# Optimization experiments

Hardware: AMD Instinct MI355X
Metric: run time of the kernel (lower is better)

## Reference

```python
import jax, jax.numpy as jnp
import numpy as np

N_HEAD, D_MODEL, D_K, D_V = 8, 256, 32, 32
LN_EPS = 1e-5

def setup_inputs() -> dict:
    key = jax.random.key(0)
    ks = jax.random.split(key, 8)
    B, L = 2, 1024
    h = jax.random.normal(ks[0], (B, L, D_MODEL), dtype=jnp.float32)
    bias = jax.random.normal(ks[1], (B, L, L, D_K), dtype=jnp.float32) * 0.02
    std_qk = np.sqrt(2.0 / (D_MODEL + D_K)).astype(np.float32)
    std_v = np.sqrt(2.0 / (D_MODEL + D_V)).astype(np.float32)
    w_qs = jax.random.normal(ks[2], (N_HEAD * D_K, D_MODEL), dtype=jnp.float32) * std_qk
    w_ks = jax.random.normal(ks[3], (N_HEAD * D_K, D_MODEL), dtype=jnp.float32) * std_qk
    w_vs = jax.random.normal(ks[4], (N_HEAD * D_V, D_MODEL), dtype=jnp.float32) * std_v
    ln_g = jnp.ones((D_MODEL,), jnp.float32)
    ln_b = jnp.zeros((D_MODEL,), jnp.float32)
    fc_w = jax.random.normal(ks[5], (D_MODEL, N_HEAD * D_V), dtype=jnp.float32) * np.sqrt(2.0 / (D_MODEL + N_HEAD * D_V)).astype(np.float32)
    fc_b = jnp.zeros((D_MODEL,), jnp.float32)
    return {"h": h, "bias": bias, "w_qs": w_qs, "w_ks": w_ks, "w_vs": w_vs,
            "ln_g": ln_g, "ln_b": ln_b, "fc_w": fc_w, "fc_b": fc_b}

def reference(h, bias, w_qs, w_ks, w_vs, ln_g, ln_b, fc_w, fc_b):
    B, L, _ = h.shape
    residual = h
    # LayerNorm
    mu = jnp.mean(h, axis=-1, keepdims=True)
    var = jnp.mean((h - mu) ** 2, axis=-1, keepdims=True)
    hn = (h - mu) * jax.lax.rsqrt(var + LN_EPS) * ln_g + ln_b
    # Projections -> (B, L, H, d)
    q = (hn @ w_qs.T).reshape(B, L, N_HEAD, D_K)
    k = (hn @ w_ks.T).reshape(B, L, N_HEAD, D_K)
    v = (hn @ w_vs.T).reshape(B, L, N_HEAD, D_V)
    # attn1: standard QK^T; attn2: per-(i,j) bias dotted with q_i (bias shared over heads)
    attn1 = jnp.einsum('bihd,bjhd->bhij', q, k)
    attn2 = jnp.einsum('bihd,bijd->bhij', q, bias)
    scores = (attn1 + attn2) / jnp.float32(np.sqrt(D_K))
    attn = jax.nn.softmax(scores, axis=-1)  # (B,H,L,L)
    emb1 = jnp.einsum('bhij,bjhd->bihd', attn, v)
    emb2 = jnp.einsum('bhij,bijd->bihd', attn, bias)
    out = (emb1 + emb2).reshape(B, L, N_HEAD * D_V)
    out = out @ fc_w.T + fc_b
    out = out + residual
    attn_ret = jnp.transpose(attn, (1, 0, 2, 3))  # (H,B,L,L) like original
    return (out, attn_ret)
```

## Files before the change

### kernel.cpp

```cpp
#include <hip/hip_runtime.h>
#include <math.h>

#define NHEAD 8
#define DMODEL 256
#define DKV 32
#define BATCH 2
#define LSEQ 1024
#define LN_EPS 1e-5f
#define INV_SQRT_DK 0.17677669529663687f

__global__ void ln_stats_kernel(const float* __restrict__ hin, float* __restrict__ stats) {
  int row = blockIdx.x;
  int t = threadIdx.x;
  float x = hin[(size_t)row * DMODEL + t];
  float s = x, ss = x * x;
#pragma unroll
  for (int off = 32; off > 0; off >>= 1) {
    s += __shfl_xor(s, off);
    ss += __shfl_xor(ss, off);
  }
  __shared__ float red[8];
  int wave = t >> 6, lane = t & 63;
  if (lane == 0) { red[wave] = s; red[4 + wave] = ss; }
  __syncthreads();
  if (t == 0) {
    float S = red[0] + red[1] + red[2] + red[3];
    float SS = red[4] + red[5] + red[6] + red[7];
    float mu = S * (1.0f / DMODEL);
    float var = SS * (1.0f / DMODEL) - mu * mu;
    stats[row * 2] = mu;
    stats[row * 2 + 1] = rsqrtf(var + LN_EPS);
  }
}

#define BM 64
#define BN 64
#define BK 16
__global__ void qkv_gemm_kernel(const float* __restrict__ hin, const float* __restrict__ stats,
                                const float* __restrict__ ln_g, const float* __restrict__ ln_b,
                                const float* __restrict__ w_qs, const float* __restrict__ w_ks,
                                const float* __restrict__ w_vs,
                                float* __restrict__ q_ws, float* __restrict__ kT,
                                float* __restrict__ vT) {
  __shared__ float As[BK][BM + 4];
  __shared__ float Bs[BK][BN + 4];
  int m0 = blockIdx.x * BM;
  int nb = blockIdx.y;
  int mat = nb >> 2;
  int n0 = (nb & 3) * BN;
  const float* W = (mat == 0) ? w_qs : (mat == 1 ? w_ks : w_vs);
  int t = threadIdx.x;
  int tx = t & 15, ty = t >> 4;
  int lr = t >> 2, lc = (t & 3) * 4;
  float mu = stats[(m0 + lr) * 2];
  float rs = stats[(m0 + lr) * 2 + 1];
  float acc[4][4] = {};
  for (int k0 = 0; k0 < DMODEL; k0 += BK) {
    __syncthreads();
    float4 a = *(const float4*)&hin[(size_t)(m0 + lr) * DMODEL + k0 + lc];
    float4 g = *(const float4*)&ln_g[k0 + lc];
    float4 bb = *(const float4*)&ln_b[k0 + lc];
    As[lc + 0][lr] = (a.x - mu) * rs * g.x + bb.x;
    As[lc + 1][lr] = (a.y - mu) * rs * g.y + bb.y;
    As[lc + 2][lr] = (a.z - mu) * rs * g.z + bb.z;
    As[lc + 3][lr] = (a.w - mu) * rs * g.w + bb.w;
    float4 w = *(const float4*)&W[(size_t)(n0 + lr) * DMODEL + k0 + lc];
    Bs[lc + 0][lr] = w.x;
    Bs[lc + 1][lr] = w.y;
    Bs[lc + 2][lr] = w.z;
    Bs[lc + 3][lr] = w.w;
    __syncthreads();
#pragma unroll
    for (int kk = 0; kk < BK; kk++) {
      float4 av = *(const float4*)&As[kk][ty * 4];
      float4 bv = *(const float4*)&Bs[kk][tx * 4];
      float am[4] = {av.x, av.y, av.z, av.w};
      float bm[4] = {bv.x, bv.y, bv.z, bv.w};
#pragma unroll
      for (int ii = 0; ii < 4; ii++)
#pragma unroll
        for (int jj = 0; jj < 4; jj++) acc[ii][jj] += am[ii] * bm[jj];
    }
  }
  if (mat == 0) {
#pragma unroll
    for (int ii = 0; ii < 4; ii++) {
      float4 st = {acc[ii][0], acc[ii][1], acc[ii][2], acc[ii][3]};
      *(float4*)&q_ws[(size_t)(m0 + ty * 4 + ii) * DMODEL + n0 + tx * 4] = st;
    }
  } else {
    float* O = (mat == 1) ? kT : vT;
    int bb2 = m0 >> 10;
    int jbase = (m0 & 1023) + ty * 4;
    float* Ob = O + (size_t)bb2 * DMODEL * LSEQ;
#pragma unroll
    for (int jj = 0; jj < 4; jj++) {
      int n = n0 + tx * 4 + jj;
      float4 st = {acc[0][jj], acc[1][jj], acc[2][jj], acc[3][jj]};
      *(float4*)&Ob[(size_t)n * LSEQ + jbase] = st;
    }
  }
}

#define JTILE 128
#define NTILE 8
#define BIASLD 132
#define BIAS_OFF 8448
#define SMEM_FLOATS (8448 + 32 * BIASLD)

__global__ __launch_bounds__(256, 3) void attn_kernel(
    const float* __restrict__ q_ws, const float* __restrict__ kT,
    const float* __restrict__ vT, const float* __restrict__ bias,
    const float* __restrict__ hin, const float* __restrict__ fc_w,
    const float* __restrict__ fc_b, float* __restrict__ out,
    float* __restrict__ attn_out) {
  __shared__ float smem[SMEM_FLOATS];
  int blk = blockIdx.x;
  int b = blk >> 10, i = blk & 1023;
  int t = threadIdx.x;
  int hh = t >> 5, jl = t & 31;
  const float* bias_row = bias + (size_t)blk * (LSEQ * DKV);
  const float* kb = kT + ((size_t)b * DMODEL + hh * DKV) * LSEQ;
  const float* vb = vT + ((size_t)b * DMODEL + hh * DKV) * LSEQ;

  float q[32];
  {
    const float4* qp = (const float4*)(q_ws + (size_t)blk * DMODEL + hh * DKV);
#pragma unroll
    for (int c = 0; c < 8; c++) {
      float4 v4 = qp[c];
      q[4 * c + 0] = v4.x; q[4 * c + 1] = v4.y;
      q[4 * c + 2] = v4.z; q[4 * c + 3] = v4.w;
    }
  }
  float acc[32];
#pragma unroll
  for (int d = 0; d < 32; d++) acc[d] = 0.f;
  float l_part = 0.f;

  float4 st[4];
#pragma unroll
  for (int c = 0; c < 4; c++)
    st[c] = *(const float4*)(bias_row + (size_t)(c * 256 + t) * 4);
#pragma unroll
  for (int c = 0; c < 4; c++) {
    int f = c * 256 + t;
    int jr = f >> 3, d0 = (f & 7) * 4;
    smem[BIAS_OFF + (d0 + 0) * BIASLD + jr] = st[c].x;
    smem[BIAS_OFF + (d0 + 1) * BIASLD + jr] = st[c].y;
    smem[BIAS_OFF + (d0 + 2) * BIASLD + jr] = st[c].z;
    smem[BIAS_OFF + (d0 + 3) * BIASLD + jr] = st[c].w;
  }
  __syncthreads();

  for (int jt = 0; jt < NTILE; jt++) {
    if (jt + 1 < NTILE) {
#pragma unroll
      for (int c = 0; c < 4; c++)
        st[c] = *(const float4*)(bias_row + (size_t)(jt + 1) * 4096 +
                                 (size_t)(c * 256 + t) * 4);
    }
    int j0 = jt * JTILE + jl * 4;
    float s0 = 0.f, s1 = 0.f, s2 = 0.f, s3 = 0.f;
#pragma unroll
    for (int d = 0; d < 32; d++) {
      float4 kv = *(const float4*)(kb + (size_t)d * LSEQ + j0);
      float4 bb = *(const float4*)&smem[BIAS_OFF + d * BIASLD + jl * 4];
      s0 += q[d] * (kv.x + bb.x);
      s1 += q[d] * (kv.y + bb.y);
      s2 += q[d] * (kv.z + bb.z);
      s3 += q[d] * (kv.w + bb.w);
    }
    float p0 = __expf(s0 * INV_SQRT_DK);
    float p1 = __expf(s1 * INV_SQRT_DK);
    float p2 = __expf(s2 * INV_SQRT_DK);
    float p3 = __expf(s3 * INV_SQRT_DK);
    l_part += (p0 + p1) + (p2 + p3);
    *(float4*)&smem[hh * 1024 + j0] = make_float4(p0, p1, p2, p3);
#pragma unroll
    for (int d = 0; d < 32; d++) {
      float4 vv = *(const float4*)(vb + (size_t)d * LSEQ + j0);
      float4 bb = *(const float4*)&smem[BIAS_OFF + d * BIASLD + jl * 4];
      acc[d] += p0 * (vv.x + bb.x) + p1 * (vv.y + bb.y) +
                p2 * (vv.z + bb.z) + p3 * (vv.w + bb.w);
    }
    __syncthreads();
    if (jt + 1 < NTILE) {
#pragma unroll
      for (int c = 0; c < 4; c++) {
        int f = c * 256 + t;
        int jr = f >> 3, d0 = (f & 7) * 4;
        smem[BIAS_OFF + (d0 + 0) * BIASLD + jr] = st[c].x;
        smem[BIAS_OFF + (d0 + 1) * BIASLD + jr] = st[c].y;
        smem[BIAS_OFF + (d0 + 2) * BIASLD + jr] = st[c].z;
        smem[BIAS_OFF + (d0 + 3) * BIASLD + jr] = st[c].w;
      }
      __syncthreads();
    }
  }

  float l = l_part;
#pragma unroll
  for (int off = 16; off > 0; off >>= 1) l += __shfl_xor(l, off);
  float inv_l = 1.0f / l;

  float* arow = attn_out + (((size_t)hh * BATCH + b) * LSEQ + i) * LSEQ;
#pragma unroll
  for (int c = 0; c < 8; c++) {
    int j0 = c * 128 + jl * 4;
    float4 pv = *(const float4*)&smem[hh * 1024 + j0];
    pv.x *= inv_l; pv.y *= inv_l; pv.z *= inv_l; pv.w *= inv_l;
    *(float4*)&arow[j0] = pv;
  }
  __syncthreads();

#pragma unroll
  for (int d = 0; d < 32; d++)
    smem[hh * 1056 + d * 33 + jl] = acc[d] * inv_l;
  __syncthreads();
  float emb = 0.f;
  {
    const float* base = &smem[(t >> 5) * 1056 + (t & 31) * 33];
#pragma unroll
    for (int r = 0; r < 32; r++) emb += base[r];
  }
  __syncthreads();
  smem[BIAS_OFF + t] = emb;
  __syncthreads();

  float o = fc_b[t];
  const float4* wrow = (const float4*)(fc_w + (size_t)t * DMODEL);
#pragma unroll
  for (int c = 0; c < 64; c++) {
    float4 wv = wrow[c];
    float4 ev = *(const float4*)&smem[BIAS_OFF + c * 4];
    o += wv.x * ev.x + wv.y * ev.y + wv.z * ev.z + wv.w * ev.w;
  }
  o += hin[(size_t)blk * DMODEL + t];
  out[(size_t)blk * DMODEL + t] = o;
}

extern "C" void kernel_launch(void* const* d_in, const int* in_sizes, int n_in,
                              void* d_out, int out_size, void* d_ws, size_t ws_size,
                              hipStream_t stream) {
  const float* h = (const float*)d_in[0];
  const float* bias = (const float*)d_in[1];
  const float* w_qs = (const float*)d_in[2];
  const float* w_ks = (const float*)d_in[3];
  const float* w_vs = (const float*)d_in[4];
  const float* ln_g = (const float*)d_in[5];
  const float* ln_b = (const float*)d_in[6];
  const float* fc_w = (const float*)d_in[7];
  const float* fc_b = (const float*)d_in[8];
  float* out = (float*)d_out;
  float* attn_out = out + (size_t)BATCH * LSEQ * DMODEL;

  float* ws = (float*)d_ws;
  float* stats = ws;
  float* q_ws = ws + 4096;
  float* kT = q_ws + (size_t)BATCH * LSEQ * DMODEL;
  float* vT = kT + (size_t)BATCH * LSEQ * DMODEL;

  ln_stats_kernel<<<BATCH * LSEQ, 256, 0, stream>>>(h, stats);
  qkv_gemm_kernel<<<dim3(32, 12), 256, 0, stream>>>(h, stats, ln_g, ln_b, w_qs, w_ks,
                                                    w_vs, q_ws, kT, vT);
  attn_kernel<<<BATCH * LSEQ, 256, 0, stream>>>(q_ws, kT, vT, bias, h, fc_w, fc_b,
                                                out, attn_out);
}
```

Before: 854.3 us.

## Double-buffer bias tiles, stage unnormalized probs in global, raise occupancy

The bias tile in shared memory becomes double-buffered: the next tile is stored into the alternate buffer after compute, so each iteration needs one barrier instead of two. Unnormalized probabilities are written straight to the attention output in global memory and rescaled in place after the softmax sum is known. This drops the 8K-float shared probability buffer and makes room for a 4-blocks-per-CU launch bound. The cost is an extra global read and write of the attention matrix, likely served mostly from cache, and tighter register limits that could cause spills.

Measured after the change: 1.538 ms. +80.0%, slower.

```diff
diff --git a/kernel.cpp b/kernel.cpp
--- a/kernel.cpp
+++ b/kernel.cpp
@@ -105,10 +105,11 @@
 #define JTILE 128
 #define NTILE 8
 #define BIASLD 132
-#define BIAS_OFF 8448
-#define SMEM_FLOATS (8448 + 32 * BIASLD)
-
-__global__ __launch_bounds__(256, 3) void attn_kernel(
+#define TILE_F (32 * BIASLD)
+#define EMB_OFF (2 * TILE_F)
+#define SMEM_FLOATS (2 * TILE_F + 256)
+
+__global__ __launch_bounds__(256, 4) void attn_kernel(
     const float* __restrict__ q_ws, const float* __restrict__ kT,
     const float* __restrict__ vT, const float* __restrict__ bias,
     const float* __restrict__ hin, const float* __restrict__ fc_w,
@@ -122,6 +123,7 @@
   const float* bias_row = bias + (size_t)blk * (LSEQ * DKV);
   const float* kb = kT + ((size_t)b * DMODEL + hh * DKV) * LSEQ;
   const float* vb = vT + ((size_t)b * DMODEL + hh * DKV) * LSEQ;
+  float* arow = attn_out + (((size_t)hh * BATCH + b) * LSEQ + i) * LSEQ;
 
   float q[32];
   {
@@ -138,34 +140,45 @@
   for (int d = 0; d < 32; d++) acc[d] = 0.f;
   float l_part = 0.f;
 
-  float4 st[4];
-#pragma unroll
-  for (int c = 0; c < 4; c++)
-    st[c] = *(const float4*)(bias_row + (size_t)(c * 256 + t) * 4);
-#pragma unroll
-  for (int c = 0; c < 4; c++) {
-    int f = c * 256 + t;
-    int jr = f >> 3, d0 = (f & 7) * 4;
-    smem[BIAS_OFF + (d0 + 0) * BIASLD + jr] = st[c].x;
-    smem[BIAS_OFF + (d0 + 1) * BIASLD + jr] = st[c].y;
-    smem[BIAS_OFF + (d0 + 2) * BIASLD + jr] = st[c].z;
-    smem[BIAS_OFF + (d0 + 3) * BIASLD + jr] = st[c].w;
+  {
+    float4 s0 = *(const float4*)(bias_row + (size_t)t * 4);
+    float4 s1 = *(const float4*)(bias_row + (size_t)(256 + t) * 4);
+    float4 s2 = *(const float4*)(bias_row + (size_t)(512 + t) * 4);
+    float4 s3 = *(const float4*)(bias_row + (size_t)(768 + t) * 4);
+    int jr, d0;
+    jr = t >> 3; d0 = (t & 7) * 4;
+    smem[(d0 + 0) * BIASLD + jr] = s0.x; smem[(d0 + 1) * BIASLD + jr] = s0.y;
+    smem[(d0 + 2) * BIASLD + jr] = s0.z; smem[(d0 + 3) * BIASLD + jr] = s0.w;
+    jr = (256 + t) >> 3; d0 = (t & 7) * 4;
+    smem[(d0 + 0) * BIASLD + jr] = s1.x; smem[(d0 + 1) * BIASLD + jr] = s1.y;
+    smem[(d0 + 2) * BIASLD + jr] = s1.z; smem[(d0 + 3) * BIASLD + jr] = s1.w;
+    jr = (512 + t) >> 3; d0 = (t & 7) * 4;
+    smem[(d0 + 0) * BIASLD + jr] = s2.x; smem[(d0 + 1) * BIASLD + jr] = s2.y;
+    smem[(d0 + 2) * BIASLD + jr] = s2.z; smem[(d0 + 3) * BIASLD + jr] = s2.w;
+    jr = (768 + t) >> 3; d0 = (t & 7) * 4;
+    smem[(d0 + 0) * BIASLD + jr] = s3.x; smem[(d0 + 1) * BIASLD + jr] = s3.y;
+    smem[(d0 + 2) * BIASLD + jr] = s3.z; smem[(d0 + 3) * BIASLD + jr] = s3.w;
   }
   __syncthreads();
 
   for (int jt = 0; jt < NTILE; jt++) {
+    const float* bufc = smem + (jt & 1) * TILE_F;
+    float4 n0, n1, n2, n3;
     if (jt + 1 < NTILE) {
-#pragma unroll
-      for (int c = 0; c < 4; c++)
-        st[c] = *(const float4*)(bias_row + (size_t)(jt + 1) * 4096 +
-                                 (size_t)(c * 256 + t) * 4);
+      const float* src = bias_row + (size_t)(jt + 1) * 4096;
+      n0 = *(const float4*)(src + (size_t)t * 4);
+      n1 = *(const float4*)(src + (size_t)(256 + t) * 4);
+      n2 = *(const float4*)(src + (size_t)(512 + t) * 4);
+      n3 = *(const float4*)(src + (size_t)(768 + t) * 4);
     }
     int j0 = jt * JTILE + jl * 4;
+    const float* kp = kb + j0;
+    const float* vp = vb + j0;
     float s0 = 0.f, s1 = 0.f, s2 = 0.f, s3 = 0.f;
 #pragma unroll
     for (int d = 0; d < 32; d++) {
-      float4 kv = *(const float4*)(kb + (size_t)d * LSEQ + j0);
-      float4 bb = *(const float4*)&smem[BIAS_OFF + d * BIASLD + jl * 4];
+      float4 kv = *(const float4*)(kp + (size_t)d * LSEQ);
+      float4 bb = *(const float4*)&bufc[d * BIASLD + jl * 4];
       s0 += q[d] * (kv.x + bb.x);
       s1 += q[d] * (kv.y + bb.y);
       s2 += q[d] * (kv.z + bb.z);
@@ -176,27 +189,31 @@
     float p2 = __expf(s2 * INV_SQRT_DK);
     float p3 = __expf(s3 * INV_SQRT_DK);
     l_part += (p0 + p1) + (p2 + p3);
-    *(float4*)&smem[hh * 1024 + j0] = make_float4(p0, p1, p2, p3);
+    *(float4*)&arow[j0] = make_float4(p0, p1, p2, p3);
 #pragma unroll
     for (int d = 0; d < 32; d++) {
-      float4 vv = *(const float4*)(vb + (size_t)d * LSEQ + j0);
-      float4 bb = *(const float4*)&smem[BIAS_OFF + d * BIASLD + jl * 4];
+      float4 vv = *(const float4*)(vp + (size_t)d * LSEQ);
+      float4 bb = *(const float4*)&bufc[d * BIASLD + jl * 4];
       acc[d] += p0 * (vv.x + bb.x) + p1 * (vv.y + bb.y) +
                 p2 * (vv.z + bb.z) + p3 * (vv.w + bb.w);
     }
+    if (jt + 1 < NTILE) {
+      float* bufn = smem + ((jt + 1) & 1) * TILE_F;
+      int jr, d0;
+      jr = t >> 3; d0 = (t & 7) * 4;
+      bufn[(d0 + 0) * BIASLD + jr] = n0.x; bufn[(d0 + 1) * BIASLD + jr] = n0.y;
+      bufn[(d0 + 2) * BIASLD + jr] = n0.z; bufn[(d0 + 3) * BIASLD + jr] = n0.w;
+      jr = (256 + t) >> 3; d0 = (t & 7) * 4;
+      bufn[(d0 + 0) * BIASLD + jr] = n1.x; bufn[(d0 + 1) * BIASLD + jr] = n1.y;
+      bufn[(d0 + 2) * BIASLD + jr] = n1.z; bufn[(d0 + 3) * BIASLD + jr] = n1.w;
+      jr = (512 + t) >> 3; d0 = (t & 7) * 4;
+      bufn[(d0 + 0) * BIASLD + jr] = n2.x; bufn[(d0 + 1) * BIASLD + jr] = n2.y;
+      bufn[(d0 + 2) * BIASLD + jr] = n2.z; bufn[(d0 + 3) * BIASLD + jr] = n2.w;
+      jr = (768 + t) >> 3; d0 = (t & 7) * 4;
+      bufn[(d0 + 0) * BIASLD + jr] = n3.x; bufn[(d0 + 1) * BIASLD + jr] = n3.y;
+      bufn[(d0 + 2) * BIASLD + jr] = n3.z; bufn[(d0 + 3) * BIASLD + jr] = n3.w;
+    }
     __syncthreads();
-    if (jt + 1 < NTILE) {
-#pragma unroll
-      for (int c = 0; c < 4; c++) {
-        int f = c * 256 + t;
-        int jr = f >> 3, d0 = (f & 7) * 4;
-        smem[BIAS_OFF + (d0 + 0) * BIASLD + jr] = st[c].x;
-        smem[BIAS_OFF + (d0 + 1) * BIASLD + jr] = st[c].y;
-        smem[BIAS_OFF + (d0 + 2) * BIASLD + jr] = st[c].z;
-        smem[BIAS_OFF + (d0 + 3) * BIASLD + jr] = st[c].w;
-      }
-      __syncthreads();
-    }
   }
 
   float l = l_part;
@@ -204,15 +221,13 @@
   for (int off = 16; off > 0; off >>= 1) l += __shfl_xor(l, off);
   float inv_l = 1.0f / l;
 
-  float* arow = attn_out + (((size_t)hh * BATCH + b) * LSEQ + i) * LSEQ;
 #pragma unroll
   for (int c = 0; c < 8; c++) {
-    int j0 = c * 128 + jl * 4;
-    float4 pv = *(const float4*)&smem[hh * 1024 + j0];
+    int jc = c * 128 + jl * 4;
+    float4 pv = *(const float4*)&arow[jc];
     pv.x *= inv_l; pv.y *= inv_l; pv.z *= inv_l; pv.w *= inv_l;
-    *(float4*)&arow[j0] = pv;
-  }
-  __syncthreads();
+    *(float4*)&arow[jc] = pv;
+  }
 
 #pragma unroll
   for (int d = 0; d < 32; d++)
@@ -225,7 +240,7 @@
     for (int r = 0; r < 32; r++) emb += base[r];
   }
   __syncthreads();
-  smem[BIAS_OFF + t] = emb;
+  smem[EMB_OFF + t] = emb;
   __syncthreads();
 
   float o = fc_b[t];
@@ -233,7 +248,7 @@
 #pragma unroll
   for (int c = 0; c < 64; c++) {
     float4 wv = wrow[c];
-    float4 ev = *(const float4*)&smem[BIAS_OFF + c * 4];
+    float4 ev = *(const float4*)&smem[EMB_OFF + c * 4];
     o += wv.x * ev.x + wv.y * ev.y + wv.z * ev.z + wv.w * ev.w;
   }
   o += hin[(size_t)blk * DMODEL + t];
```
